# Kernel tuning notes

Measured on AMD Instinct MI355X. Metric: run time of the kernel, lower is better.

The kernel has to match this reference:

```python
import jax, jax.numpy as jnp
import numpy as np

N = 40000
E = 640000
DIN = 128
H = 128
G = 16
C = 10


def setup_inputs() -> dict:
    key = jax.random.key(0)
    ks = jax.random.split(key, 12)
    x = jax.random.normal(ks[0], (N, DIN), dtype=jnp.float32)
    edge_index = jax.random.randint(ks[1], (2, E), 0, N, dtype=jnp.int64)
    batch = jnp.sort(jax.random.randint(ks[2], (N,), 0, G, dtype=jnp.int64))
    s = 1.0 / np.sqrt(H)
    W_in = jax.random.normal(ks[3], (DIN, H), dtype=jnp.float32) * s
    b_in = jnp.zeros((H,), dtype=jnp.float32)
    W1 = jax.random.normal(ks[4], (H, H), dtype=jnp.float32) * s
    b1 = jnp.zeros((H,), dtype=jnp.float32)
    W2 = jax.random.normal(ks[5], (H, H), dtype=jnp.float32) * s
    b2 = jnp.zeros((H,), dtype=jnp.float32)
    Wf1 = jax.random.normal(ks[6], (H, H // 2), dtype=jnp.float32) * s
    bf1 = jnp.zeros((H // 2,), dtype=jnp.float32)
    Wf2 = jax.random.normal(ks[7], (H // 2, C), dtype=jnp.float32) * (1.0 / np.sqrt(H // 2))
    bf2 = jnp.zeros((C,), dtype=jnp.float32)
    return {"x": x, "edge_index": edge_index, "batch": batch,
            "W_in": W_in, "b_in": b_in, "W1": W1, "b1": b1,
            "W2": W2, "b2": b2, "Wf1": Wf1, "bf1": bf1,
            "Wf2": Wf2, "bf2": bf2}


def _gcn_conv(h, src, dst, deg_inv_sqrt, W, b):
    # h' = D^{-1/2} (A + I) D^{-1/2} (h W) + b  (PyG GCNConv with self-loops)
    hw = h @ W  # [N, H]
    norm = deg_inv_sqrt[src] * deg_inv_sqrt[dst]  # [E]
    agg = jax.ops.segment_sum(hw[src] * norm[:, None], dst, num_segments=N)
    agg = agg + hw * (deg_inv_sqrt * deg_inv_sqrt)[:, None]  # self-loop term
    return agg + b


def reference(x, edge_index, batch, W_in, b_in, W1, b1, W2, b2, Wf1, bf1, Wf2, bf2):
    src, dst = edge_index[0], edge_index[1]
    # degree on target nodes, including self-loop (+1)
    deg = jax.ops.segment_sum(jnp.ones((E,), dtype=x.dtype), dst, num_segments=N) + 1.0
    deg_inv_sqrt = jax.lax.rsqrt(deg)

    h = x @ W_in + b_in
    h = jax.nn.relu(_gcn_conv(h, src, dst, deg_inv_sqrt, W1, b1))  # dropout is identity in eval
    h = jax.nn.relu(_gcn_conv(h, src, dst, deg_inv_sqrt, W2, b2))

    # global mean pool by graph id
    sums = jax.ops.segment_sum(h, batch, num_segments=G)  # [G, H]
    counts = jax.ops.segment_sum(jnp.ones((N,), dtype=h.dtype), batch, num_segments=G)
    pooled = sums / jnp.maximum(counts, 1.0)[:, None]

    out = jax.nn.relu(pooled @ Wf1 + bf1) @ Wf2 + bf2  # [G, C]
    return out
```

## Files before the change

kernel.cpp:

```cpp
#include <hip/hip_runtime.h>
#include <hip/hip_fp16.h>

#define NN 40000
#define EE 640000
#define NCH 157

typedef unsigned int uint;
typedef unsigned short ushort;
typedef __attribute__((ext_vector_type(8))) short short8;
typedef __attribute__((ext_vector_type(4))) float floatx4;
typedef __attribute__((ext_vector_type(4))) uint uint4e;

__device__ inline ushort f2bf(float f) {
    uint u = __float_as_uint(f);
    return (ushort)((u + 0x7fffu + ((u >> 16) & 1u)) >> 16);
}
__device__ inline float bf_lo(uint u) { return __uint_as_float(u << 16); }
__device__ inline float bf_hi(uint u) { return __uint_as_float(u & 0xffff0000u); }

__device__ inline int lower_bound_dev(const int* __restrict__ a, int n, int x) {
    int lo = 0, hi = n;
    while (lo < hi) { int m = (lo + hi) >> 1; if (a[m] < x) lo = m + 1; else hi = m; }
    return lo;
}

__global__ __launch_bounds__(256) void histprep_kernel(const int* __restrict__ dst,
                                                       int* __restrict__ counts,
                                                       const float* __restrict__ W_in,
                                                       const float* __restrict__ W1,
                                                       const float* __restrict__ b_in,
                                                       const float* __restrict__ W2,
                                                       const int* __restrict__ batch,
                                                       ushort* __restrict__ Bp1,
                                                       ushort* __restrict__ Bp2,
                                                       float* __restrict__ cvec,
                                                       int* __restrict__ glo) {
    int b = blockIdx.x, t = threadIdx.x;
    if (b < 2500) {
        atomicAdd(&counts[dst[b * 256 + t]], 1);
    } else if (b < 2564) {
        int idx = (b - 2500) * 256 + t;
        int k = idx >> 7, n = idx & 127;
        float s = 0.f;
        for (int j = 0; j < 128; ++j) s = fmaf(W_in[k * 128 + j], W1[j * 128 + n], s);
        Bp1[((size_t)(k >> 3) * 128 + n) * 8 + (k & 7)] = f2bf(s);
    } else if (b < 2628) {
        int idx = (b - 2564) * 256 + t;
        int k = idx >> 7, n = idx & 127;
        Bp2[((size_t)(k >> 3) * 128 + n) * 8 + (k & 7)] = f2bf(W2[idx]);
    } else {
        if (t < 128) {
            float s = 0.f;
            for (int k = 0; k < 128; ++k) s = fmaf(b_in[k], W1[k * 128 + t], s);
            cvec[t] = s;
        } else if (t < 128 + 17) {
            int g = t - 128;
            glo[g] = lower_bound_dev(batch, NN, g);
        }
    }
}

__global__ __launch_bounds__(256) void scan_kernel(const int* __restrict__ counts,
                                                   int* __restrict__ goff,
                                                   int* __restrict__ start,
                                                   int* __restrict__ cursor,
                                                   float* __restrict__ dis,
                                                   uint* __restrict__ spack, int N) {
    __shared__ int ws[4];
    __shared__ int sbase;
    int t = threadIdx.x, lane = t & 63, wv = t >> 6;
    int idx = blockIdx.x * 256 + t;
    int c = (idx < N) ? counts[idx] : 0;
    int v = c;
    #pragma unroll
    for (int d = 1; d < 64; d <<= 1) {
        int u = __shfl_up(v, d, 64);
        if (lane >= d) v += u;
    }
    if (lane == 63) ws[wv] = v;
    __syncthreads();
    if (t == 0) {
        int total = ws[0] + ws[1] + ws[2] + ws[3];
        sbase = atomicAdd(goff, total);
    }
    __syncthreads();
    int off = sbase;
    for (int j = 0; j < wv; ++j) off += ws[j];
    if (idx < N) {
        int excl = off + v - c;
        start[idx] = excl;
        cursor[idx] = excl;
        float dv = rsqrtf((float)c + 1.0f);
        dis[idx] = dv;
        spack[idx] = (uint)idx | ((uint)__half_as_ushort(__float2half_rn(dv)) << 16);
    }
}

template <bool ABF16>
__device__ inline void mm_tile(const void* __restrict__ Av, const ushort* __restrict__ Bpack,
                               ushort* __restrict__ C, int tile, int wv, int lane) {
    int m = lane & 15, q = lane >> 4;
    int row = tile * 64 + wv * 16 + m;

    short8 afr[4];
    if (ABF16) {
        const ushort* A = (const ushort*)Av;
        const ushort* ap = A + (size_t)row * 128 + q * 8;
        #pragma unroll
        for (int k0 = 0; k0 < 4; ++k0) afr[k0] = *(const short8*)(ap + k0 * 32);
    } else {
        const float* A = (const float*)Av;
        const float* ap = A + (size_t)row * 128 + q * 8;
        #pragma unroll
        for (int k0 = 0; k0 < 4; ++k0) {
            float4 f0 = *(const float4*)(ap + k0 * 32);
            float4 f1 = *(const float4*)(ap + k0 * 32 + 4);
            short8 a;
            a[0] = (short)f2bf(f0.x); a[1] = (short)f2bf(f0.y);
            a[2] = (short)f2bf(f0.z); a[3] = (short)f2bf(f0.w);
            a[4] = (short)f2bf(f1.x); a[5] = (short)f2bf(f1.y);
            a[6] = (short)f2bf(f1.z); a[7] = (short)f2bf(f1.w);
            afr[k0] = a;
        }
    }

    floatx4 acc[8];
    #pragma unroll
    for (int nt = 0; nt < 8; ++nt) { floatx4 z = {0.f, 0.f, 0.f, 0.f}; acc[nt] = z; }

    #pragma unroll
    for (int nt = 0; nt < 8; ++nt) {
        #pragma unroll
        for (int k0 = 0; k0 < 4; ++k0) {
            short8 bfrag = *(const short8*)(Bpack + ((size_t)(k0 * 4 + q) * 128 + nt * 16 + m) * 8);
            acc[nt] = __builtin_amdgcn_mfma_f32_16x16x32_bf16(afr[k0], bfrag, acc[nt], 0, 0, 0);
        }
    }

    int orow_base = tile * 64 + wv * 16 + q * 4;
    #pragma unroll
    for (int nt = 0; nt < 8; ++nt) {
        #pragma unroll
        for (int r = 0; r < 4; ++r)
            C[(size_t)(orow_base + r) * 128 + nt * 16 + m] = f2bf(acc[nt][r]);
    }
}

__global__ __launch_bounds__(256) void fillmm1_kernel(const int* __restrict__ src,
                                                      const int* __restrict__ dst,
                                                      const uint* __restrict__ spack,
                                                      int* __restrict__ cursor,
                                                      uint* __restrict__ edata,
                                                      const float* __restrict__ x,
                                                      const ushort* __restrict__ Bp1,
                                                      ushort* __restrict__ bufA) {
    int b = blockIdx.x, t = threadIdx.x;
    if (b < 2500) {
        int e = b * 256 + t;
        int s = src[e], d = dst[e];
        int pos = atomicAdd(&cursor[d], 1);
        edata[pos] = spack[s];
    } else {
        mm_tile<false>(x, Bp1, bufA, b - 2500, t >> 6, t & 63);
    }
}

__global__ __launch_bounds__(256) void agg1m_kernel(const ushort* __restrict__ hw,
                                                    const float* __restrict__ dis,
                                                    const int* __restrict__ start,
                                                    const int* __restrict__ counts,
                                                    const uint* __restrict__ edata,
                                                    const float* __restrict__ cvec,
                                                    const float* __restrict__ bias,
                                                    const ushort* __restrict__ Bp2,
                                                    ushort* __restrict__ C) {
    __shared__ ushort Atile[16][128];
    __shared__ uint eds[4][64];
    int t = threadIdx.x;
    int wv = t >> 6, lane = t & 63;
    int qg = lane & 15, h4 = lane >> 4;
    const uint4* __restrict__ hv4 = (const uint4*)hw;
    int base = blockIdx.x * 16;
    char* abase = (char*)&Atile[0][0];

    for (int n = 0; n < 4; ++n) {
        int nl = wv * 4 + n;
        int i = base + nl;
        int beg = start[i];
        int deg = counts[i];
        int dmain = deg > 64 ? 64 : deg;

        uint ed;
        if (lane < dmain) ed = edata[beg + lane];
        else ed = (uint)i;
        eds[wv][lane] = ed;

        float a0 = 0.f, a1 = 0.f, a2 = 0.f, a3 = 0.f;
        float a4 = 0.f, a5 = 0.f, a6 = 0.f, a7 = 0.f;
        float sn = 0.f;

        int dpad = (dmain + 15) & ~15;
        for (int j = 0; j < dpad; j += 16) {
            uint e0 = eds[wv][j + h4];
            uint e1 = eds[wv][j + 4 + h4];
            uint e2 = eds[wv][j + 8 + h4];
            uint e3 = eds[wv][j + 12 + h4];
            uint4 u0 = hv4[(size_t)(e0 & 0xffffu) * 16 + qg];
            uint4 u1 = hv4[(size_t)(e1 & 0xffffu) * 16 + qg];
            uint4 u2 = hv4[(size_t)(e2 & 0xffffu) * 16 + qg];
            uint4 u3 = hv4[(size_t)(e3 & 0xffffu) * 16 + qg];
            float n0 = __half2float(__ushort_as_half((ushort)(e0 >> 16)));
            float n1 = __half2float(__ushort_as_half((ushort)(e1 >> 16)));
            float n2 = __half2float(__ushort_as_half((ushort)(e2 >> 16)));
            float n3 = __half2float(__ushort_as_half((ushort)(e3 >> 16)));
            a0 = fmaf(n0, bf_lo(u0.x), a0); a1 = fmaf(n0, bf_hi(u0.x), a1);
            a2 = fmaf(n0, bf_lo(u0.y), a2); a3 = fmaf(n0, bf_hi(u0.y), a3);
            a4 = fmaf(n0, bf_lo(u0.z), a4); a5 = fmaf(n0, bf_hi(u0.z), a5);
            a6 = fmaf(n0, bf_lo(u0.w), a6); a7 = fmaf(n0, bf_hi(u0.w), a7);
            a0 = fmaf(n1, bf_lo(u1.x), a0); a1 = fmaf(n1, bf_hi(u1.x), a1);
            a2 = fmaf(n1, bf_lo(u1.y), a2); a3 = fmaf(n1, bf_hi(u1.y), a3);
            a4 = fmaf(n1, bf_lo(u1.z), a4); a5 = fmaf(n1, bf_hi(u1.z), a5);
            a6 = fmaf(n1, bf_lo(u1.w), a6); a7 = fmaf(n1, bf_hi(u1.w), a7);
            a0 = fmaf(n2, bf_lo(u2.x), a0); a1 = fmaf(n2, bf_hi(u2.x), a1);
            a2 = fmaf(n2, bf_lo(u2.y), a2); a3 = fmaf(n2, bf_hi(u2.y), a3);
            a4 = fmaf(n2, bf_lo(u2.z), a4); a5 = fmaf(n2, bf_hi(u2.z), a5);
            a6 = fmaf(n2, bf_lo(u2.w), a6); a7 = fmaf(n2, bf_hi(u2.w), a7);
            a0 = fmaf(n3, bf_lo(u3.x), a0); a1 = fmaf(n3, bf_hi(u3.x), a1);
            a2 = fmaf(n3, bf_lo(u3.y), a2); a3 = fmaf(n3, bf_hi(u3.y), a3);
            a4 = fmaf(n3, bf_lo(u3.z), a4); a5 = fmaf(n3, bf_hi(u3.z), a5);
            a6 = fmaf(n3, bf_lo(u3.w), a6); a7 = fmaf(n3, bf_hi(u3.w), a7);
            sn += (n0 + n1) + (n2 + n3);
        }
        for (int e = beg + 64; e < beg + deg; ++e) {
            uint et = edata[e];
            if (h4 == 0) {
                float n0 = __half2float(__ushort_as_half((ushort)(et >> 16)));
                uint4 u = hv4[(size_t)(et & 0xffffu) * 16 + qg];
                a0 = fmaf(n0, bf_lo(u.x), a0); a1 = fmaf(n0, bf_hi(u.x), a1);
                a2 = fmaf(n0, bf_lo(u.y), a2); a3 = fmaf(n0, bf_hi(u.y), a3);
                a4 = fmaf(n0, bf_lo(u.z), a4); a5 = fmaf(n0, bf_hi(u.z), a5);
                a6 = fmaf(n0, bf_lo(u.w), a6); a7 = fmaf(n0, bf_hi(u.w), a7);
                sn += n0;
            }
        }

        a0 += __shfl_xor(a0, 16); a0 += __shfl_xor(a0, 32);
        a1 += __shfl_xor(a1, 16); a1 += __shfl_xor(a1, 32);
        a2 += __shfl_xor(a2, 16); a2 += __shfl_xor(a2, 32);
        a3 += __shfl_xor(a3, 16); a3 += __shfl_xor(a3, 32);
        a4 += __shfl_xor(a4, 16); a4 += __shfl_xor(a4, 32);
        a5 += __shfl_xor(a5, 16); a5 += __shfl_xor(a5, 32);
        a6 += __shfl_xor(a6, 16); a6 += __shfl_xor(a6, 32);
        a7 += __shfl_xor(a7, 16); a7 += __shfl_xor(a7, 32);
        sn += __shfl_xor(sn, 16); sn += __shfl_xor(sn, 32);

        float di = dis[i];
        float sii = di * di;
        a0 *= di; a1 *= di; a2 *= di; a3 *= di;
        a4 *= di; a5 *= di; a6 *= di; a7 *= di;
        sn *= di;
        uint4 su = hv4[(size_t)i * 16 + qg];
        a0 = fmaf(sii, bf_lo(su.x), a0); a1 = fmaf(sii, bf_hi(su.x), a1);
        a2 = fmaf(sii, bf_lo(su.y), a2); a3 = fmaf(sii, bf_hi(su.y), a3);
        a4 = fmaf(sii, bf_lo(su.z), a4); a5 = fmaf(sii, bf_hi(su.z), a5);
        a6 = fmaf(sii, bf_lo(su.w), a6); a7 = fmaf(sii, bf_hi(su.w), a7);
        sn += sii;

        float4 ca = *(const float4*)(cvec + 8 * qg);
        float4 cb = *(const float4*)(cvec + 8 * qg + 4);
        float4 ba = *(const float4*)(bias + 8 * qg);
        float4 bb = *(const float4*)(bias + 8 * qg + 4);
        float o0 = fmaxf(fmaf(sn, ca.x, a0) + ba.x, 0.f);
        float o1 = fmaxf(fmaf(sn, ca.y, a1) + ba.y, 0.f);
        float o2 = fmaxf(fmaf(sn, ca.z, a2) + ba.z, 0.f);
        float o3 = fmaxf(fmaf(sn, ca.w, a3) + ba.w, 0.f);
        float o4 = fmaxf(fmaf(sn, cb.x, a4) + bb.x, 0.f);
        float o5 = fmaxf(fmaf(sn, cb.y, a5) + bb.y, 0.f);
        float o6 = fmaxf(fmaf(sn, cb.z, a6) + bb.z, 0.f);
        float o7 = fmaxf(fmaf(sn, cb.w, a7) + bb.w, 0.f);

        if (h4 == 0) {
            uint4e o;
            o.x = (uint)f2bf(o0) | ((uint)f2bf(o1) << 16);
            o.y = (uint)f2bf(o2) | ((uint)f2bf(o3) << 16);
            o.z = (uint)f2bf(o4) | ((uint)f2bf(o5) << 16);
            o.w = (uint)f2bf(o6) | ((uint)f2bf(o7) << 16);
            int slot = qg ^ (nl & 7);
            *(uint4e*)(abase + nl * 256 + slot * 16) = o;
        }
    }

    __syncthreads();

    {
        int m = lane & 15, qm = lane >> 4;
        short8 afr[4];
        #pragma unroll
        for (int k0 = 0; k0 < 4; ++k0) {
            int slot = (qm + 4 * k0) ^ (m & 7);
            afr[k0] = *(const short8*)(abase + m * 256 + slot * 16);
        }
        floatx4 acc[2];
        #pragma unroll
        for (int u = 0; u < 2; ++u) { floatx4 z = {0.f, 0.f, 0.f, 0.f}; acc[u] = z; }
        #pragma unroll
        for (int u = 0; u < 2; ++u) {
            int nt = 2 * wv + u;
            #pragma unroll
            for (int k0 = 0; k0 < 4; ++k0) {
                short8 bfrag = *(const short8*)(Bp2 + ((size_t)(k0 * 4 + qm) * 128 + nt * 16 + m) * 8);
                acc[u] = __builtin_amdgcn_mfma_f32_16x16x32_bf16(afr[k0], bfrag, acc[u], 0, 0, 0);
            }
        }
        int orow_base = base + qm * 4;
        #pragma unroll
        for (int u = 0; u < 2; ++u) {
            int nt = 2 * wv + u;
            #pragma unroll
            for (int r = 0; r < 4; ++r)
                C[(size_t)(orow_base + r) * 128 + nt * 16 + m] = f2bf(acc[u][r]);
        }
    }
}

__global__ __launch_bounds__(256) void agg_kernel(const ushort* __restrict__ hw,
                                                  const float* __restrict__ dis,
                                                  const int* __restrict__ start,
                                                  const int* __restrict__ counts,
                                                  const uint* __restrict__ edata,
                                                  const float* __restrict__ cvec,
                                                  const float* __restrict__ bias,
                                                  ushort* __restrict__ out, int N) {
    __shared__ uint eds[4][64];
    int wv = threadIdx.x >> 6;
    int lane = threadIdx.x & 63;
    int q = lane & 15, h4 = lane >> 4;
    int i = blockIdx.x * 4 + wv;
    if (i >= N) return;
    int beg = start[i];
    int deg = counts[i];
    int dmain = deg > 64 ? 64 : deg;
    const uint4* __restrict__ hv4 = (const uint4*)hw;

    uint ed;
    if (lane < dmain) ed = edata[beg + lane];
    else ed = (uint)i;
    eds[wv][lane] = ed;

    float a0 = 0.f, a1 = 0.f, a2 = 0.f, a3 = 0.f;
    float a4 = 0.f, a5 = 0.f, a6 = 0.f, a7 = 0.f;
    float sn = 0.f;

    int dpad = (dmain + 15) & ~15;
    for (int j = 0; j < dpad; j += 16) {
        uint e0 = eds[wv][j + h4];
        uint e1 = eds[wv][j + 4 + h4];
        uint e2 = eds[wv][j + 8 + h4];
        uint e3 = eds[wv][j + 12 + h4];
        uint4 u0 = hv4[(size_t)(e0 & 0xffffu) * 16 + q];
        uint4 u1 = hv4[(size_t)(e1 & 0xffffu) * 16 + q];
        uint4 u2 = hv4[(size_t)(e2 & 0xffffu) * 16 + q];
        uint4 u3 = hv4[(size_t)(e3 & 0xffffu) * 16 + q];
        float n0 = __half2float(__ushort_as_half((ushort)(e0 >> 16)));
        float n1 = __half2float(__ushort_as_half((ushort)(e1 >> 16)));
        float n2 = __half2float(__ushort_as_half((ushort)(e2 >> 16)));
        float n3 = __half2float(__ushort_as_half((ushort)(e3 >> 16)));
        a0 = fmaf(n0, bf_lo(u0.x), a0); a1 = fmaf(n0, bf_hi(u0.x), a1);
        a2 = fmaf(n0, bf_lo(u0.y), a2); a3 = fmaf(n0, bf_hi(u0.y), a3);
        a4 = fmaf(n0, bf_lo(u0.z), a4); a5 = fmaf(n0, bf_hi(u0.z), a5);
        a6 = fmaf(n0, bf_lo(u0.w), a6); a7 = fmaf(n0, bf_hi(u0.w), a7);
        a0 = fmaf(n1, bf_lo(u1.x), a0); a1 = fmaf(n1, bf_hi(u1.x), a1);
        a2 = fmaf(n1, bf_lo(u1.y), a2); a3 = fmaf(n1, bf_hi(u1.y), a3);
        a4 = fmaf(n1, bf_lo(u1.z), a4); a5 = fmaf(n1, bf_hi(u1.z), a5);
        a6 = fmaf(n1, bf_lo(u1.w), a6); a7 = fmaf(n1, bf_hi(u1.w), a7);
        a0 = fmaf(n2, bf_lo(u2.x), a0); a1 = fmaf(n2, bf_hi(u2.x), a1);
        a2 = fmaf(n2, bf_lo(u2.y), a2); a3 = fmaf(n2, bf_hi(u2.y), a3);
        a4 = fmaf(n2, bf_lo(u2.z), a4); a5 = fmaf(n2, bf_hi(u2.z), a5);
        a6 = fmaf(n2, bf_lo(u2.w), a6); a7 = fmaf(n2, bf_hi(u2.w), a7);
        a0 = fmaf(n3, bf_lo(u3.x), a0); a1 = fmaf(n3, bf_hi(u3.x), a1);
        a2 = fmaf(n3, bf_lo(u3.y), a2); a3 = fmaf(n3, bf_hi(u3.y), a3);
        a4 = fmaf(n3, bf_lo(u3.z), a4); a5 = fmaf(n3, bf_hi(u3.z), a5);
        a6 = fmaf(n3, bf_lo(u3.w), a6); a7 = fmaf(n3, bf_hi(u3.w), a7);
        sn += (n0 + n1) + (n2 + n3);
    }
    for (int e = beg + 64; e < beg + deg; ++e) {
        uint et = edata[e];
        if (h4 == 0) {
            float n0 = __half2float(__ushort_as_half((ushort)(et >> 16)));
            uint4 u = hv4[(size_t)(et & 0xffffu) * 16 + q];
            a0 = fmaf(n0, bf_lo(u.x), a0); a1 = fmaf(n0, bf_hi(u.x), a1);
            a2 = fmaf(n0, bf_lo(u.y), a2); a3 = fmaf(n0, bf_hi(u.y), a3);
            a4 = fmaf(n0, bf_lo(u.z), a4); a5 = fmaf(n0, bf_hi(u.z), a5);
            a6 = fmaf(n0, bf_lo(u.w), a6); a7 = fmaf(n0, bf_hi(u.w), a7);
            sn += n0;
        }
    }

    a0 += __shfl_xor(a0, 16); a0 += __shfl_xor(a0, 32);
    a1 += __shfl_xor(a1, 16); a1 += __shfl_xor(a1, 32);
    a2 += __shfl_xor(a2, 16); a2 += __shfl_xor(a2, 32);
    a3 += __shfl_xor(a3, 16); a3 += __shfl_xor(a3, 32);
    a4 += __shfl_xor(a4, 16); a4 += __shfl_xor(a4, 32);
    a5 += __shfl_xor(a5, 16); a5 += __shfl_xor(a5, 32);
    a6 += __shfl_xor(a6, 16); a6 += __shfl_xor(a6, 32);
    a7 += __shfl_xor(a7, 16); a7 += __shfl_xor(a7, 32);
    sn += __shfl_xor(sn, 16); sn += __shfl_xor(sn, 32);

    float di = dis[i];
    float sii = di * di;
    a0 *= di; a1 *= di; a2 *= di; a3 *= di;
    a4 *= di; a5 *= di; a6 *= di; a7 *= di;
    sn *= di;
    uint4 su = hv4[(size_t)i * 16 + q];
    a0 = fmaf(sii, bf_lo(su.x), a0); a1 = fmaf(sii, bf_hi(su.x), a1);
    a2 = fmaf(sii, bf_lo(su.y), a2); a3 = fmaf(sii, bf_hi(su.y), a3);
    a4 = fmaf(sii, bf_lo(su.z), a4); a5 = fmaf(sii, bf_hi(su.z), a5);
    a6 = fmaf(sii, bf_lo(su.w), a6); a7 = fmaf(sii, bf_hi(su.w), a7);
    sn += sii;

    float c0 = 0.f, c1 = 0.f, c2 = 0.f, c3 = 0.f;
    float c4 = 0.f, c5 = 0.f, c6 = 0.f, c7 = 0.f;
    if (cvec) {
        float4 ca = *(const float4*)(cvec + 8 * q);
        float4 cb = *(const float4*)(cvec + 8 * q + 4);
        c0 = ca.x; c1 = ca.y; c2 = ca.z; c3 = ca.w;
        c4 = cb.x; c5 = cb.y; c6 = cb.z; c7 = cb.w;
    }
    float4 ba = *(const float4*)(bias + 8 * q);
    float4 bb = *(const float4*)(bias + 8 * q + 4);
    float o0 = fmaxf(fmaf(sn, c0, a0) + ba.x, 0.f);
    float o1 = fmaxf(fmaf(sn, c1, a1) + ba.y, 0.f);
    float o2 = fmaxf(fmaf(sn, c2, a2) + ba.z, 0.f);
    float o3 = fmaxf(fmaf(sn, c3, a3) + ba.w, 0.f);
    float o4 = fmaxf(fmaf(sn, c4, a4) + bb.x, 0.f);
    float o5 = fmaxf(fmaf(sn, c5, a5) + bb.y, 0.f);
    float o6 = fmaxf(fmaf(sn, c6, a6) + bb.z, 0.f);
    float o7 = fmaxf(fmaf(sn, c7, a7) + bb.w, 0.f);
    if (h4 == 0) {
        uint4 o;
        o.x = (uint)f2bf(o0) | ((uint)f2bf(o1) << 16);
        o.y = (uint)f2bf(o2) | ((uint)f2bf(o3) << 16);
        o.z = (uint)f2bf(o4) | ((uint)f2bf(o5) << 16);
        o.w = (uint)f2bf(o6) | ((uint)f2bf(o7) << 16);
        ((uint4*)out)[(size_t)i * 16 + q] = o;
    }
}

__global__ __launch_bounds__(256) void pool_kernel(const ushort* __restrict__ h,
                                                   const int* __restrict__ glo,
                                                   float* __restrict__ pools) {
    int t = threadIdx.x, c2 = t & 63, wv = t >> 6;
    int b = blockIdx.x;
    int g = b >> 6, ch = b & 63;
    int lo = glo[g], hi = glo[g + 1];
    int span = hi - lo;
    int chunk = (span + 63) >> 6;
    int r0 = lo + ch * chunk;
    int r1 = hi < r0 + chunk ? hi : r0 + chunk;
    const uint* __restrict__ hv = (const uint*)h;

    float a0 = 0.f, a1 = 0.f;
    #pragma unroll 4
    for (int j = r0 + wv; j < r1; j += 4) {
        uint u = hv[(size_t)j * 64 + c2];
        a0 += bf_lo(u);
        a1 += bf_hi(u);
    }
    if (r0 < r1) {
        atomicAdd(&pools[g * 128 + 2 * c2], a0);
        atomicAdd(&pools[g * 128 + 2 * c2 + 1], a1);
    }
}

__global__ __launch_bounds__(256) void final_kernel(const int* __restrict__ glo,
                                                    const float* __restrict__ pools,
                                                    const float* __restrict__ Wf1,
                                                    const float* __restrict__ bf1,
                                                    const float* __restrict__ Wf2,
                                                    const float* __restrict__ bf2,
                                                    float* __restrict__ out) {
    __shared__ float pooled[16][128];
    __shared__ float z[16][64];
    int t = threadIdx.x;
    for (int idx = t; idx < 2048; idx += 256) {
        int gg = idx >> 7, c = idx & 127;
        int cn = glo[gg + 1] - glo[gg];
        float cnf = (float)(cn > 1 ? cn : 1);
        pooled[gg][c] = pools[idx] / cnf;
    }
    __syncthreads();
    for (int idx = t; idx < 1024; idx += 256) {
        int gg = idx >> 6, j = idx & 63;
        float s = bf1[j];
        for (int k = 0; k < 128; ++k) s = fmaf(pooled[gg][k], Wf1[k * 64 + j], s);
        z[gg][j] = fmaxf(s, 0.f);
    }
    __syncthreads();
    if (t < 160) {
        int gg = t / 10, k = t % 10;
        float s = bf2[k];
        for (int j = 0; j < 64; ++j) s = fmaf(z[gg][j], Wf2[j * 10 + k], s);
        out[t] = s;
    }
}


extern "C" void kernel_launch(void* const* d_in, const int* in_sizes, int n_in,
                              void* d_out, int out_size, void* d_ws, size_t ws_size,
                              hipStream_t stream) {
    const float* x    = (const float*)d_in[0];
    const int* edge   = (const int*)d_in[1];
    const int* batch  = (const int*)d_in[2];
    const float* W_in = (const float*)d_in[3];
    const float* b_in = (const float*)d_in[4];
    const float* W1   = (const float*)d_in[5];
    const float* b1   = (const float*)d_in[6];
    const float* W2   = (const float*)d_in[7];
    const float* b2   = (const float*)d_in[8];
    const float* Wf1  = (const float*)d_in[9];
    const float* bf1  = (const float*)d_in[10];
    const float* Wf2  = (const float*)d_in[11];
    const float* bf2  = (const float*)d_in[12];
    float* out = (float*)d_out;

    char* ws = (char*)d_ws;
    size_t off = 0;
    auto alloc = [&](size_t bytes) -> void* {
        void* p = ws + off;
        off += (bytes + 511) & ~(size_t)511;
        return p;
    };
    int* counts   = (int*)alloc((size_t)NN * 4);
    float* pools  = (float*)alloc(16 * 128 * 4);
    int* misc     = (int*)alloc(512);
    size_t zero_bytes = off;
    int* goff     = misc;
    int* glo      = misc + 8;
    ushort* bufA  = (ushort*)alloc((size_t)NN * 128 * 2);
    ushort* bufB  = (ushort*)alloc((size_t)NN * 128 * 2);
    ushort* bufC  = (ushort*)alloc((size_t)NN * 128 * 2);
    ushort* Bp1   = (ushort*)alloc(128 * 128 * 2);
    ushort* Bp2   = (ushort*)alloc(128 * 128 * 2);
    float* cvec   = (float*)alloc(128 * 4);
    float* dis    = (float*)alloc((size_t)NN * 4);
    uint* spack   = (uint*)alloc((size_t)NN * 4);
    int* start    = (int*)alloc((size_t)NN * 4);
    int* cursor   = (int*)alloc((size_t)NN * 4);
    uint* edata   = (uint*)alloc((size_t)EE * 4);

    hipMemsetAsync(counts, 0, zero_bytes, stream);

    histprep_kernel<<<2629, 256, 0, stream>>>(edge + EE, counts, W_in, W1, b_in, W2,
                                              batch, Bp1, Bp2, cvec, glo);
    scan_kernel<<<NCH, 256, 0, stream>>>(counts, goff, start, cursor, dis, spack, NN);
    fillmm1_kernel<<<2500 + NN / 64, 256, 0, stream>>>(edge, edge + EE, spack, cursor,
                                                       edata, x, Bp1, bufA);
    agg1m_kernel<<<NN / 16, 256, 0, stream>>>(bufA, dis, start, counts, edata,
                                              cvec, b1, Bp2, bufC);
    agg_kernel<<<NN / 4, 256, 0, stream>>>(bufC, dis, start, counts, edata, nullptr, b2, bufB, NN);
    pool_kernel<<<1024, 256, 0, stream>>>(bufB, glo, pools);
    final_kernel<<<1, 256, 0, stream>>>(glo, pools, Wf1, bf1, Wf2, bf2, out);
}
```

Before: 243.9 us.

## Replace CSR build with fixed-size per-node buckets and overflow list

Builds the adjacency as fixed 64-slot per-destination buckets of 16-bit source ids filled in one atomic pass, removing the separate histogram and prefix-scan kernels. Edges beyond 64 per node go to a global overflow list that aggregation scans linearly. Normalisation is now fetched via spack gather at aggregation time. Pool kernel also reduces in shared memory before global atomics. Risks slow linear overflow scan for high-degree nodes and an extra indirect load per edge.

```diff
diff --git a/kernel.cpp b/kernel.cpp
--- a/kernel.cpp
+++ b/kernel.cpp
@@ -24,28 +24,24 @@
     return lo;
 }
 
-__global__ __launch_bounds__(256) void histprep_kernel(const int* __restrict__ dst,
-                                                       int* __restrict__ counts,
-                                                       const float* __restrict__ W_in,
-                                                       const float* __restrict__ W1,
-                                                       const float* __restrict__ b_in,
-                                                       const float* __restrict__ W2,
-                                                       const int* __restrict__ batch,
-                                                       ushort* __restrict__ Bp1,
-                                                       ushort* __restrict__ Bp2,
-                                                       float* __restrict__ cvec,
-                                                       int* __restrict__ glo) {
+__global__ __launch_bounds__(256) void prep_kernel(const float* __restrict__ W_in,
+                                                   const float* __restrict__ W1,
+                                                   const float* __restrict__ b_in,
+                                                   const float* __restrict__ W2,
+                                                   const int* __restrict__ batch,
+                                                   ushort* __restrict__ Bp1,
+                                                   ushort* __restrict__ Bp2,
+                                                   float* __restrict__ cvec,
+                                                   int* __restrict__ glo) {
     int b = blockIdx.x, t = threadIdx.x;
-    if (b < 2500) {
-        atomicAdd(&counts[dst[b * 256 + t]], 1);
-    } else if (b < 2564) {
-        int idx = (b - 2500) * 256 + t;
+    if (b < 64) {
+        int idx = b * 256 + t;
         int k = idx >> 7, n = idx & 127;
         float s = 0.f;
         for (int j = 0; j < 128; ++j) s = fmaf(W_in[k * 128 + j], W1[j * 128 + n], s);
         Bp1[((size_t)(k >> 3) * 128 + n) * 8 + (k & 7)] = f2bf(s);
-    } else if (b < 2628) {
-        int idx = (b - 2564) * 256 + t;
+    } else if (b < 128) {
+        int idx = (b - 64) * 256 + t;
         int k = idx >> 7, n = idx & 127;
         Bp2[((size_t)(k >> 3) * 128 + n) * 8 + (k & 7)] = f2bf(W2[idx]);
     } else {
@@ -60,42 +56,6 @@
     }
 }
 
-__global__ __launch_bounds__(256) void scan_kernel(const int* __restrict__ counts,
-                                                   int* __restrict__ goff,
-                                                   int* __restrict__ start,
-                                                   int* __restrict__ cursor,
-                                                   float* __restrict__ dis,
-                                                   uint* __restrict__ spack, int N) {
-    __shared__ int ws[4];
-    __shared__ int sbase;
-    int t = threadIdx.x, lane = t & 63, wv = t >> 6;
-    int idx = blockIdx.x * 256 + t;
-    int c = (idx < N) ? counts[idx] : 0;
-    int v = c;
-    #pragma unroll
-    for (int d = 1; d < 64; d <<= 1) {
-        int u = __shfl_up(v, d, 64);
-        if (lane >= d) v += u;
-    }
-    if (lane == 63) ws[wv] = v;
-    __syncthreads();
-    if (t == 0) {
-        int total = ws[0] + ws[1] + ws[2] + ws[3];
-        sbase = atomicAdd(goff, total);
-    }
-    __syncthreads();
-    int off = sbase;
-    for (int j = 0; j < wv; ++j) off += ws[j];
-    if (idx < N) {
-        int excl = off + v - c;
-        start[idx] = excl;
-        cursor[idx] = excl;
-        float dv = rsqrtf((float)c + 1.0f);
-        dis[idx] = dv;
-        spack[idx] = (uint)idx | ((uint)__half_as_ushort(__float2half_rn(dv)) << 16);
-    }
-}
-
 template <bool ABF16>
 __device__ inline void mm_tile(const void* __restrict__ Av, const ushort* __restrict__ Bpack,
                                ushort* __restrict__ C, int tile, int wv, int lane) {
@@ -146,30 +106,49 @@
     }
 }
 
-__global__ __launch_bounds__(256) void fillmm1_kernel(const int* __restrict__ src,
-                                                      const int* __restrict__ dst,
-                                                      const uint* __restrict__ spack,
-                                                      int* __restrict__ cursor,
-                                                      uint* __restrict__ edata,
-                                                      const float* __restrict__ x,
-                                                      const ushort* __restrict__ Bp1,
-                                                      ushort* __restrict__ bufA) {
+__global__ __launch_bounds__(256) void fill_kernel(const int* __restrict__ src,
+                                                   const int* __restrict__ dst,
+                                                   int* __restrict__ cnt,
+                                                   int* __restrict__ ovfcnt,
+                                                   uint* __restrict__ ovf,
+                                                   ushort* __restrict__ bucket,
+                                                   const float* __restrict__ x,
+                                                   const ushort* __restrict__ Bp1,
+                                                   ushort* __restrict__ bufA) {
     int b = blockIdx.x, t = threadIdx.x;
     if (b < 2500) {
         int e = b * 256 + t;
         int s = src[e], d = dst[e];
-        int pos = atomicAdd(&cursor[d], 1);
-        edata[pos] = spack[s];
+        int pos = atomicAdd(&cnt[d], 1);
+        if (pos < 64) {
+            bucket[(size_t)d * 64 + pos] = (ushort)s;
+        } else {
+            int k = atomicAdd(ovfcnt, 1);
+            ovf[k] = (uint)d | ((uint)s << 16);
+        }
     } else {
         mm_tile<false>(x, Bp1, bufA, b - 2500, t >> 6, t & 63);
     }
 }
 
+__global__ __launch_bounds__(256) void dsprep_kernel(const int* __restrict__ cnt,
+                                                     float* __restrict__ dis,
+                                                     uint* __restrict__ spack, int N) {
+    int i = blockIdx.x * 256 + threadIdx.x;
+    if (i < N) {
+        float dv = rsqrtf((float)cnt[i] + 1.0f);
+        dis[i] = dv;
+        spack[i] = (uint)i | ((uint)__half_as_ushort(__float2half_rn(dv)) << 16);
+    }
+}
+
 __global__ __launch_bounds__(256) void agg1m_kernel(const ushort* __restrict__ hw,
                                                     const float* __restrict__ dis,
-                                                    const int* __restrict__ start,
-                                                    const int* __restrict__ counts,
-                                                    const uint* __restrict__ edata,
+                                                    const int* __restrict__ cnt,
+                                                    const ushort* __restrict__ bucket,
+                                                    const uint* __restrict__ spack,
+                                                    const uint* __restrict__ ovf,
+                                                    const int* __restrict__ ovfcnt,
                                                     const float* __restrict__ cvec,
                                                     const float* __restrict__ bias,
                                                     const ushort* __restrict__ Bp2,
@@ -186,13 +165,11 @@
     for (int n = 0; n < 4; ++n) {
         int nl = wv * 4 + n;
         int i = base + nl;
-        int beg = start[i];
-        int deg = counts[i];
+        int deg = cnt[i];
         int dmain = deg > 64 ? 64 : deg;
 
-        uint ed;
-        if (lane < dmain) ed = edata[beg + lane];
-        else ed = (uint)i;
+        uint ed = (uint)i;
+        if (lane < dmain) ed = spack[bucket[(size_t)i * 64 + lane]];
         eds[wv][lane] = ed;
 
         float a0 = 0.f, a1 = 0.f, a2 = 0.f, a3 = 0.f;
@@ -231,16 +208,21 @@
             a6 = fmaf(n3, bf_lo(u3.w), a6); a7 = fmaf(n3, bf_hi(u3.w), a7);
             sn += (n0 + n1) + (n2 + n3);
         }
-        for (int e = beg + 64; e < beg + deg; ++e) {
-            uint et = edata[e];
-            if (h4 == 0) {
-                float n0 = __half2float(__ushort_as_half((ushort)(et >> 16)));
-                uint4 u = hv4[(size_t)(et & 0xffffu) * 16 + qg];
-                a0 = fmaf(n0, bf_lo(u.x), a0); a1 = fmaf(n0, bf_hi(u.x), a1);
-                a2 = fmaf(n0, bf_lo(u.y), a2); a3 = fmaf(n0, bf_hi(u.y), a3);
-                a4 = fmaf(n0, bf_lo(u.z), a4); a5 = fmaf(n0, bf_hi(u.z), a5);
-                a6 = fmaf(n0, bf_lo(u.w), a6); a7 = fmaf(n0, bf_hi(u.w), a7);
-                sn += n0;
+        if (deg > 64) {
+            int ovfn = *ovfcnt;
+            for (int k = 0; k < ovfn; ++k) {
+                uint oe = ovf[k];
+                if ((int)(oe & 0xffffu) == i && h4 == 0) {
+                    int s2 = (int)(oe >> 16);
+                    uint sp = spack[s2];
+                    float n0 = __half2float(__ushort_as_half((ushort)(sp >> 16)));
+                    uint4 u = hv4[(size_t)s2 * 16 + qg];
+                    a0 = fmaf(n0, bf_lo(u.x), a0); a1 = fmaf(n0, bf_hi(u.x), a1);
+                    a2 = fmaf(n0, bf_lo(u.y), a2); a3 = fmaf(n0, bf_hi(u.y), a3);
+                    a4 = fmaf(n0, bf_lo(u.z), a4); a5 = fmaf(n0, bf_hi(u.z), a5);
+                    a6 = fmaf(n0, bf_lo(u.w), a6); a7 = fmaf(n0, bf_hi(u.w), a7);
+                    sn += n0;
+                }
             }
         }
 
@@ -325,9 +307,11 @@
 
 __global__ __launch_bounds__(256) void agg_kernel(const ushort* __restrict__ hw,
                                                   const float* __restrict__ dis,
-                                                  const int* __restrict__ start,
-                                                  const int* __restrict__ counts,
-                                                  const uint* __restrict__ edata,
+                                                  const int* __restrict__ cnt,
+                                                  const ushort* __restrict__ bucket,
+                                                  const uint* __restrict__ spack,
+                                                  const uint* __restrict__ ovf,
+                                                  const int* __restrict__ ovfcnt,
                                                   const float* __restrict__ cvec,
                                                   const float* __restrict__ bias,
                                                   ushort* __restrict__ out, int N) {
@@ -337,14 +321,12 @@
     int q = lane & 15, h4 = lane >> 4;
     int i = blockIdx.x * 4 + wv;
     if (i >= N) return;
-    int beg = start[i];
-    int deg = counts[i];
+    int deg = cnt[i];
     int dmain = deg > 64 ? 64 : deg;
     const uint4* __restrict__ hv4 = (const uint4*)hw;
 
-    uint ed;
-    if (lane < dmain) ed = edata[beg + lane];
-    else ed = (uint)i;
+    uint ed = (uint)i;
+    if (lane < dmain) ed = spack[bucket[(size_t)i * 64 + lane]];
     eds[wv][lane] = ed;
 
     float a0 = 0.f, a1 = 0.f, a2 = 0.f, a3 = 0.f;
@@ -383,16 +365,21 @@
         a6 = fmaf(n3, bf_lo(u3.w), a6); a7 = fmaf(n3, bf_hi(u3.w), a7);
         sn += (n0 + n1) + (n2 + n3);
     }
-    for (int e = beg + 64; e < beg + deg; ++e) {
-        uint et = edata[e];
-        if (h4 == 0) {
-            float n0 = __half2float(__ushort_as_half((ushort)(et >> 16)));
-            uint4 u = hv4[(size_t)(et & 0xffffu) * 16 + q];
-            a0 = fmaf(n0, bf_lo(u.x), a0); a1 = fmaf(n0, bf_hi(u.x), a1);
-            a2 = fmaf(n0, bf_lo(u.y), a2); a3 = fmaf(n0, bf_hi(u.y), a3);
-            a4 = fmaf(n0, bf_lo(u.z), a4); a5 = fmaf(n0, bf_hi(u.z), a5);
-            a6 = fmaf(n0, bf_lo(u.w), a6); a7 = fmaf(n0, bf_hi(u.w), a7);
-            sn += n0;
+    if (deg > 64) {
+        int ovfn = *ovfcnt;
+        for (int k = 0; k < ovfn; ++k) {
+            uint oe = ovf[k];
+            if ((int)(oe & 0xffffu) == i && h4 == 0) {
+                int s2 = (int)(oe >> 16);
+                uint sp = spack[s2];
+                float n0 = __half2float(__ushort_as_half((ushort)(sp >> 16)));
+                uint4 u = hv4[(size_t)s2 * 16 + q];
+                a0 = fmaf(n0, bf_lo(u.x), a0); a1 = fmaf(n0, bf_hi(u.x), a1);
+                a2 = fmaf(n0, bf_lo(u.y), a2); a3 = fmaf(n0, bf_hi(u.y), a3);
+                a4 = fmaf(n0, bf_lo(u.z), a4); a5 = fmaf(n0, bf_hi(u.z), a5);
+                a6 = fmaf(n0, bf_lo(u.w), a6); a7 = fmaf(n0, bf_hi(u.w), a7);
+                sn += n0;
+            }
         }
     }
 
@@ -449,6 +436,7 @@
 __global__ __launch_bounds__(256) void pool_kernel(const ushort* __restrict__ h,
                                                    const int* __restrict__ glo,
                                                    float* __restrict__ pools) {
+    __shared__ float spool[128];
     int t = threadIdx.x, c2 = t & 63, wv = t >> 6;
     int b = blockIdx.x;
     int g = b >> 6, ch = b & 63;
@@ -459,6 +447,9 @@
     int r1 = hi < r0 + chunk ? hi : r0 + chunk;
     const uint* __restrict__ hv = (const uint*)h;
 
+    if (t < 128) spool[t] = 0.f;
+    __syncthreads();
+
     float a0 = 0.f, a1 = 0.f;
     #pragma unroll 4
     for (int j = r0 + wv; j < r1; j += 4) {
@@ -467,8 +458,13 @@
         a1 += bf_hi(u);
     }
     if (r0 < r1) {
-        atomicAdd(&pools[g * 128 + 2 * c2], a0);
-        atomicAdd(&pools[g * 128 + 2 * c2 + 1], a1);
+        atomicAdd(&spool[2 * c2], a0);
+        atomicAdd(&spool[2 * c2 + 1], a1);
+    }
+    __syncthreads();
+    if (t < 128) {
+        float v = spool[t];
+        if (v != 0.f) atomicAdd(&pools[g * 128 + t], v);
     }
 }
 
@@ -530,11 +526,11 @@
         off += (bytes + 511) & ~(size_t)511;
         return p;
     };
-    int* counts   = (int*)alloc((size_t)NN * 4);
+    int* cnt      = (int*)alloc((size_t)NN * 4);
     float* pools  = (float*)alloc(16 * 128 * 4);
     int* misc     = (int*)alloc(512);
     size_t zero_bytes = off;
-    int* goff     = misc;
+    int* ovfcnt   = misc;
     int* glo      = misc + 8;
     ushort* bufA  = (ushort*)alloc((size_t)NN * 128 * 2);
     ushort* bufB  = (ushort*)alloc((size_t)NN * 128 * 2);
@@ -544,20 +540,19 @@
     float* cvec   = (float*)alloc(128 * 4);
     float* dis    = (float*)alloc((size_t)NN * 4);
     uint* spack   = (uint*)alloc((size_t)NN * 4);
-    int* start    = (int*)alloc((size_t)NN * 4);
-    int* cursor   = (int*)alloc((size_t)NN * 4);
-    uint* edata   = (uint*)alloc((size_t)EE * 4);
-
-    hipMemsetAsync(counts, 0, zero_bytes, stream);
-
-    histprep_kernel<<<2629, 256, 0, stream>>>(edge + EE, counts, W_in, W1, b_in, W2,
-                                              batch, Bp1, Bp2, cvec, glo);
-    scan_kernel<<<NCH, 256, 0, stream>>>(counts, goff, start, cursor, dis, spack, NN);
-    fillmm1_kernel<<<2500 + NN / 64, 256, 0, stream>>>(edge, edge + EE, spack, cursor,
-                                                       edata, x, Bp1, bufA);
-    agg1m_kernel<<<NN / 16, 256, 0, stream>>>(bufA, dis, start, counts, edata,
+    ushort* bucket= (ushort*)alloc((size_t)NN * 64 * 2);
+    uint* ovf     = (uint*)alloc((size_t)EE * 4);
+
+    hipMemsetAsync(cnt, 0, zero_bytes, stream);
+
+    prep_kernel<<<129, 256, 0, stream>>>(W_in, W1, b_in, W2, batch, Bp1, Bp2, cvec, glo);
+    fill_kernel<<<2500 + NN / 64, 256, 0, stream>>>(edge, edge + EE, cnt, ovfcnt, ovf,
+                                                    bucket, x, Bp1, bufA);
+    dsprep_kernel<<<NCH, 256, 0, stream>>>(cnt, dis, spack, NN);
+    agg1m_kernel<<<NN / 16, 256, 0, stream>>>(bufA, dis, cnt, bucket, spack, ovf, ovfcnt,
                                               cvec, b1, Bp2, bufC);
-    agg_kernel<<<NN / 4, 256, 0, stream>>>(bufC, dis, start, counts, edata, nullptr, b2, bufB, NN);
+    agg_kernel<<<NN / 4, 256, 0, stream>>>(bufC, dis, cnt, bucket, spack, ovf, ovfcnt,
+                                           nullptr, b2, bufB, NN);
     pool_kernel<<<1024, 256, 0, stream>>>(bufB, glo, pools);
     final_kernel<<<1, 256, 0, stream>>>(glo, pools, Wf1, bf1, Wf2, bf2, out);
 }
```

Result: faster. 221.7 us (-9.1%).
